# Kernel optimization log

Hardware: AMD Instinct MI355X
Metric: run time of the kernel (lower is better)

The kernel has to match this reference:

```python
import jax, jax.numpy as jnp
import numpy as np

# Class weights from __init__: total/len_i with len_0=1000, len_1=3000, len_2=6000
_TOTAL = 1000.0 + 3000.0 + 6000.0
CLASS_WEIGHTS = jnp.array([_TOTAL / 1000.0, _TOTAL / 3000.0, _TOTAL / 6000.0], dtype=jnp.float32)
NUM_CLASSES = 3
SMOOTHING = 0.1


def setup_inputs() -> dict:
    key = jax.random.key(0)
    k1, k2 = jax.random.split(key)
    N = 8388608
    pred = jax.random.normal(k1, (N, NUM_CLASSES), dtype=jnp.float32)
    label = jax.random.randint(k2, (N,), 0, NUM_CLASSES, dtype=jnp.int64)
    return {"pred": pred, "label": label}


def reference(pred, label):
    # log(softmax(pred)) computed stably; same math as -log(softmax) in the original
    logp = jax.nn.log_softmax(pred, axis=1)                      # [N, 3]
    one_hot = jax.nn.one_hot(label, NUM_CLASSES, dtype=pred.dtype)  # [N, 3]
    smoothed = (1.0 - SMOOTHING) * one_hot + SMOOTHING / NUM_CLASSES
    per_sample = -jnp.sum(logp * smoothed, axis=-1)              # [N]
    w = CLASS_WEIGHTS[label]                                     # gather per-sample weight
    return jnp.sum(per_sample * w) / pred.shape[0]
```

## Files before the change

kernel.cpp:

```cpp
#include <hip/hip_runtime.h>

#define NBLOCKS 2048
#define NTHREADS 256

__device__ __forceinline__ float wave_reduce_sum(float v) {
    #pragma unroll
    for (int off = 32; off > 0; off >>= 1)
        v += __shfl_down(v, off, 64);
    return v;
}

__device__ __forceinline__ float sample_loss(float p0, float p1, float p2, int lab) {
    float m = fmaxf(p0, fmaxf(p1, p2));
    float e = __expf(p0 - m) + __expf(p1 - m) + __expf(p2 - m);
    float lse = m + __logf(e);
    float pl = (lab == 0) ? p0 : ((lab == 1) ? p1 : p2);
    float w  = (lab == 0) ? 10.0f : ((lab == 1) ? (10.0f / 3.0f) : (10.0f / 6.0f));
    float per = lse - (0.1f / 3.0f) * (p0 + p1 + p2) - 0.9f * pl;
    return w * per;
}

__global__ void __launch_bounds__(NTHREADS, 8)
ce_partial_kernel(const float* __restrict__ pred,
                  const int* __restrict__ label,
                  float* __restrict__ partials, int n) {
    int tid = blockIdx.x * blockDim.x + threadIdx.x;
    int nthreads = gridDim.x * blockDim.x;
    int groups = n >> 2;
    float acc = 0.0f;

    for (int g = tid; g < groups; g += nthreads) {
        const float4* p4 = reinterpret_cast<const float4*>(pred + (size_t)g * 12);
        float4 a = p4[0];
        float4 b = p4[1];
        float4 c = p4[2];
        int4 l = reinterpret_cast<const int4*>(label)[g];
        acc += sample_loss(a.x, a.y, a.z, l.x);
        acc += sample_loss(a.w, b.x, b.y, l.y);
        acc += sample_loss(b.z, b.w, c.x, l.z);
        acc += sample_loss(c.y, c.z, c.w, l.w);
    }
    if (tid == 0) {
        for (int i = groups << 2; i < n; ++i) {
            acc += sample_loss(pred[(size_t)i * 3], pred[(size_t)i * 3 + 1],
                               pred[(size_t)i * 3 + 2], label[i]);
        }
    }

    __shared__ float sdata[NTHREADS / 64];
    float wsum = wave_reduce_sum(acc);
    int lane = threadIdx.x & 63;
    int wid = threadIdx.x >> 6;
    if (lane == 0) sdata[wid] = wsum;
    __syncthreads();
    if (threadIdx.x == 0) {
        float s = 0.0f;
        #pragma unroll
        for (int i = 0; i < NTHREADS / 64; ++i) s += sdata[i];
        partials[blockIdx.x] = s;
    }
}

__global__ void __launch_bounds__(256)
ce_final_kernel(const float* __restrict__ partials, int nparts,
                float* __restrict__ out, float inv_n) {
    float acc = 0.0f;
    for (int i = threadIdx.x; i < nparts; i += 256) acc += partials[i];
    __shared__ float sdata[4];
    float wsum = wave_reduce_sum(acc);
    int lane = threadIdx.x & 63;
    int wid = threadIdx.x >> 6;
    if (lane == 0) sdata[wid] = wsum;
    __syncthreads();
    if (threadIdx.x == 0) {
        float s = sdata[0] + sdata[1] + sdata[2] + sdata[3];
        out[0] = s * inv_n;
    }
}

extern "C" void kernel_launch(void* const* d_in, const int* in_sizes, int n_in,
                              void* d_out, int out_size, void* d_ws, size_t ws_size,
                              hipStream_t stream) {
    const float* pred = (const float*)d_in[0];
    const int* label = (const int*)d_in[1];
    int n = in_sizes[1];
    float* partials = (float*)d_ws;
    float* out = (float*)d_out;

    ce_partial_kernel<<<NBLOCKS, NTHREADS, 0, stream>>>(pred, label, partials, n);
    ce_final_kernel<<<1, 256, 0, stream>>>(partials, NBLOCKS, out, 1.0f / (float)n);
}
```

Before: 29.34 us.

## Stage coalesced tile loads through LDS with register prefetch of next tile

Each block now loads 1024-sample tiles with fully coalesced float4 reads, one contiguous vector per thread, and stages them in shared memory. It prefetches the next tile into registers while computing on the current one. This replaces the strided per-thread 48-byte group reads, aiming for better coalescing and more memory-level overlap. The final reduction also becomes a single 64-thread wave with vector loads. Costs are extra LDS traffic, two barriers per tile, and possible bank conflicts from the stride-3 LDS reads.

```diff
diff --git a/kernel.cpp b/kernel.cpp
--- a/kernel.cpp
+++ b/kernel.cpp
@@ -2,6 +2,10 @@
 
 #define NBLOCKS 2048
 #define NTHREADS 256
+#define TILE 1024
+
+typedef float __attribute__((ext_vector_type(4))) fx4;
+typedef int   __attribute__((ext_vector_type(4))) ix4;
 
 __device__ __forceinline__ float wave_reduce_sum(float v) {
     #pragma unroll
@@ -24,36 +28,58 @@
 ce_partial_kernel(const float* __restrict__ pred,
                   const int* __restrict__ label,
                   float* __restrict__ partials, int n) {
-    int tid = blockIdx.x * blockDim.x + threadIdx.x;
-    int nthreads = gridDim.x * blockDim.x;
-    int groups = n >> 2;
+    __shared__ float sp[3 * TILE];
+    __shared__ int   sl[TILE];
+    __shared__ float sdata[NTHREADS / 64];
+
+    const int t = threadIdx.x;
+    const int ntiles = n >> 10;
     float acc = 0.0f;
 
-    for (int g = tid; g < groups; g += nthreads) {
-        const float4* p4 = reinterpret_cast<const float4*>(pred + (size_t)g * 12);
-        float4 a = p4[0];
-        float4 b = p4[1];
-        float4 c = p4[2];
-        int4 l = reinterpret_cast<const int4*>(label)[g];
-        acc += sample_loss(a.x, a.y, a.z, l.x);
-        acc += sample_loss(a.w, b.x, b.y, l.y);
-        acc += sample_loss(b.z, b.w, c.x, l.z);
-        acc += sample_loss(c.y, c.z, c.w, l.w);
+    fx4 r0, r1, r2; ix4 rl;
+    int tile = blockIdx.x;
+    if (tile < ntiles) {
+        const fx4* p4 = reinterpret_cast<const fx4*>(pred + (size_t)tile * (3 * TILE));
+        r0 = p4[t];
+        r1 = p4[t + 256];
+        r2 = p4[t + 512];
+        rl = reinterpret_cast<const ix4*>(label + (size_t)tile * TILE)[t];
     }
-    if (tid == 0) {
-        for (int i = groups << 2; i < n; ++i) {
+    while (tile < ntiles) {
+        int next = tile + gridDim.x;
+        reinterpret_cast<fx4*>(sp)[t]       = r0;
+        reinterpret_cast<fx4*>(sp)[t + 256] = r1;
+        reinterpret_cast<fx4*>(sp)[t + 512] = r2;
+        reinterpret_cast<ix4*>(sl)[t]       = rl;
+        __syncthreads();
+        if (next < ntiles) {
+            const fx4* p4 = reinterpret_cast<const fx4*>(pred + (size_t)next * (3 * TILE));
+            r0 = p4[t];
+            r1 = p4[t + 256];
+            r2 = p4[t + 512];
+            rl = reinterpret_cast<const ix4*>(label + (size_t)next * TILE)[t];
+        }
+        #pragma unroll
+        for (int k = 0; k < 4; ++k) {
+            int s = t + (k << 8);
+            acc += sample_loss(sp[3 * s], sp[3 * s + 1], sp[3 * s + 2], sl[s]);
+        }
+        __syncthreads();
+        tile = next;
+    }
+    if (blockIdx.x == 0 && t == 0) {
+        for (int i = ntiles << 10; i < n; ++i) {
             acc += sample_loss(pred[(size_t)i * 3], pred[(size_t)i * 3 + 1],
                                pred[(size_t)i * 3 + 2], label[i]);
         }
     }
 
-    __shared__ float sdata[NTHREADS / 64];
     float wsum = wave_reduce_sum(acc);
-    int lane = threadIdx.x & 63;
-    int wid = threadIdx.x >> 6;
+    int lane = t & 63;
+    int wid  = t >> 6;
     if (lane == 0) sdata[wid] = wsum;
     __syncthreads();
-    if (threadIdx.x == 0) {
+    if (t == 0) {
         float s = 0.0f;
         #pragma unroll
         for (int i = 0; i < NTHREADS / 64; ++i) s += sdata[i];
@@ -61,21 +87,17 @@
     }
 }
 
-__global__ void __launch_bounds__(256)
-ce_final_kernel(const float* __restrict__ partials, int nparts,
-                float* __restrict__ out, float inv_n) {
-    float acc = 0.0f;
-    for (int i = threadIdx.x; i < nparts; i += 256) acc += partials[i];
-    __shared__ float sdata[4];
-    float wsum = wave_reduce_sum(acc);
-    int lane = threadIdx.x & 63;
-    int wid = threadIdx.x >> 6;
-    if (lane == 0) sdata[wid] = wsum;
-    __syncthreads();
-    if (threadIdx.x == 0) {
-        float s = sdata[0] + sdata[1] + sdata[2] + sdata[3];
-        out[0] = s * inv_n;
-    }
+__global__ void __launch_bounds__(64)
+ce_final_kernel(const float* __restrict__ partials, float* __restrict__ out,
+                float inv_n) {
+    int l = threadIdx.x;
+    fx4 s4 = {0.0f, 0.0f, 0.0f, 0.0f};
+    #pragma unroll
+    for (int k = 0; k < 8; ++k)
+        s4 += reinterpret_cast<const fx4*>(partials)[l + (k << 6)];
+    float v = s4.x + s4.y + s4.z + s4.w;
+    v = wave_reduce_sum(v);
+    if (l == 0) out[0] = v * inv_n;
 }
 
 extern "C" void kernel_launch(void* const* d_in, const int* in_sizes, int n_in,
@@ -88,5 +110,5 @@
     float* out = (float*)d_out;
 
     ce_partial_kernel<<<NBLOCKS, NTHREADS, 0, stream>>>(pred, label, partials, n);
-    ce_final_kernel<<<1, 256, 0, stream>>>(partials, NBLOCKS, out, 1.0f / (float)n);
+    ce_final_kernel<<<1, 64, 0, stream>>>(partials, out, 1.0f / (float)n);
 }
```

Result: faster. 28.11 us (-4.2%).
